# Kernel tuning notes

Hardware: AMD Instinct MI355X
Metric: run time of the kernel (lower is better)

Reference implementation:

```python
import jax, jax.numpy as jnp
import numpy as np

B, T, C = 2, 2048, 1024
LAT = 256
N_HEAD = 16
HEAD_DIM = C // N_HEAD
SCALE = 1.0 / np.sqrt(HEAD_DIM).astype(np.float32)


def setup_inputs() -> dict:
    key = jax.random.key(0)
    ks = jax.random.split(key, 9)
    s_in = 0.02  # small init so softmax is well-conditioned
    return {
        "x": jax.random.normal(ks[0], (B, T, C), dtype=jnp.float32),
        "wq_lat": jax.random.normal(ks[1], (C, LAT), dtype=jnp.float32) * s_in,
        "wk_lat": jax.random.normal(ks[2], (C, LAT), dtype=jnp.float32) * s_in,
        "wv_lat": jax.random.normal(ks[3], (C, LAT), dtype=jnp.float32) * s_in,
        "wq_heads": jax.random.normal(ks[4], (LAT, C), dtype=jnp.float32) * s_in,
        "wk_heads": jax.random.normal(ks[5], (LAT, C), dtype=jnp.float32) * s_in,
        "wv_heads": jax.random.normal(ks[6], (LAT, C), dtype=jnp.float32) * s_in,
        "w_proj": jax.random.normal(ks[7], (C, C), dtype=jnp.float32) * s_in,
        "b_proj": jnp.zeros((C,), dtype=jnp.float32),
    }


def reference(x, wq_lat, wk_lat, wv_lat, wq_heads, wk_heads, wv_heads, w_proj, b_proj):
    Bx, Tx, Cx = x.shape
    # low-rank latent projections then up-projection to per-head q/k/v
    q = (x @ wq_lat) @ wq_heads  # [B,T,C]
    k = (x @ wk_lat) @ wk_heads
    v = (x @ wv_lat) @ wv_heads
    q = q.reshape(Bx, Tx, N_HEAD, HEAD_DIM).transpose(0, 2, 1, 3)  # [B,H,T,D]
    k = k.reshape(Bx, Tx, N_HEAD, HEAD_DIM).transpose(0, 2, 1, 3)
    v = v.reshape(Bx, Tx, N_HEAD, HEAD_DIM).transpose(0, 2, 1, 3)
    att = jnp.einsum("bhqd,bhkd->bhqk", q, k) * SCALE  # [B,H,T,T]
    causal = jnp.tril(jnp.ones((Tx, Tx), dtype=bool))
    att = jnp.where(causal[None, None], att, -jnp.inf)
    att = jax.nn.softmax(att, axis=-1)
    y = jnp.einsum("bhqk,bhkd->bhqd", att, v)  # [B,H,T,D]
    y = y.transpose(0, 2, 1, 3).reshape(Bx, Tx, Cx)
    return y @ w_proj + b_proj
```

## Files before the change

### kernel.cpp

```cpp
#include <hip/hip_runtime.h>

#define SCALE 0.125f
#define SL 0.18033688011112042f

typedef __bf16 bf16x8 __attribute__((ext_vector_type(8)));
typedef short short4v __attribute__((ext_vector_type(4)));
typedef unsigned short u16x4 __attribute__((ext_vector_type(4)));
typedef float f32x4 __attribute__((ext_vector_type(4)));
typedef unsigned int uint2v __attribute__((ext_vector_type(2)));

__device__ __forceinline__ unsigned short f2b(float f) {
  unsigned u = __float_as_uint(f);
  u += 0x7fffu + ((u >> 16) & 1u);
  return (unsigned short)(u >> 16);
}
__device__ __forceinline__ float ex2(float x) {
  float r;
  asm("v_exp_f32 %0, %1" : "=v"(r) : "v"(x));
  return r;
}

#define GLB(p) ((__attribute__((address_space(1))) void*)(void*)(p))
#define LDSP(p) ((__attribute__((address_space(3))) void*)(p))

__global__ __launch_bounds__(256) void prep(
    const float* __restrict__ x, const float* __restrict__ wq_lat,
    const float* __restrict__ wk_lat, const float* __restrict__ wv_lat,
    const float* __restrict__ wq_h, const float* __restrict__ wk_h,
    const float* __restrict__ wv_h, const float* __restrict__ w_proj,
    unsigned short* __restrict__ x_bf, unsigned short* __restrict__ wlatT,
    unsigned short* __restrict__ whT, unsigned short* __restrict__ wpT) {
  __shared__ float tile[32][33];
  const int blk = blockIdx.x, tid = threadIdx.x;
  if (blk < 1024) {
    int i = blk * 256 + tid;
#pragma unroll
    for (int j = 0; j < 4; j++) {
      float4 v = ((const float4*)x)[i + j * 262144];
      u16x4 p;
      p.x = f2b(v.x); p.y = f2b(v.y); p.z = f2b(v.z); p.w = f2b(v.w);
      ((u16x4*)x_bf)[i + j * 262144] = p;
    }
  } else if (blk < 1792) {
    int idx = blk - 1024;
    int z = idx >> 8, rem = idx & 255;
    const float* wsrc = z == 0 ? wq_lat : (z == 1 ? wk_lat : wv_lat);
    unsigned short* o = wlatT + z * 262144;
    int c0 = (rem & 7) * 32, r0 = (rem >> 3) * 32;
    int tx = tid & 31, ty = tid >> 5;
#pragma unroll
    for (int i = 0; i < 32; i += 8) tile[ty + i][tx] = wsrc[(r0 + ty + i) * 256 + c0 + tx];
    __syncthreads();
#pragma unroll
    for (int i = 0; i < 32; i += 8) o[(c0 + ty + i) * 1024 + r0 + tx] = f2b(tile[tx][ty + i]);
  } else if (blk < 2560) {
    int idx = blk - 1792;
    int z = idx >> 8, rem = idx & 255;
    const float* wsrc = z == 0 ? wq_h : (z == 1 ? wk_h : wv_h);
    unsigned short* o = whT + z * 262144;
    int c0 = (rem & 31) * 32, r0 = (rem >> 5) * 32;
    int tx = tid & 31, ty = tid >> 5;
#pragma unroll
    for (int i = 0; i < 32; i += 8) tile[ty + i][tx] = wsrc[(r0 + ty + i) * 1024 + c0 + tx];
    __syncthreads();
#pragma unroll
    for (int i = 0; i < 32; i += 8) o[(c0 + ty + i) * 256 + r0 + tx] = f2b(tile[tx][ty + i]);
  } else {
    int idx = blk - 2560;
    int c0 = (idx & 31) * 32, r0 = (idx >> 5) * 32;
    int tx = tid & 31, ty = tid >> 5;
#pragma unroll
    for (int i = 0; i < 32; i += 8) tile[ty + i][tx] = w_proj[(r0 + ty + i) * 1024 + c0 + tx];
    __syncthreads();
#pragma unroll
    for (int i = 0; i < 32; i += 8) wpT[(c0 + ty + i) * 1024 + r0 + tx] = f2b(tile[tx][ty + i]);
  }
}

template <int MODE>
__global__ __launch_bounds__(256) void gemm_bt(
    const unsigned short* __restrict__ A0, const unsigned short* __restrict__ A1,
    const unsigned short* __restrict__ A2,
    const unsigned short* __restrict__ B0, const unsigned short* __restrict__ B1,
    const unsigned short* __restrict__ B2,
    void* __restrict__ C0, void* __restrict__ C1, void* __restrict__ C2,
    const float* __restrict__ bias, int M, int N, int K) {
  int bx, by, z;
  if (gridDim.y == 1) {
    const int lin = blockIdx.x;
    const int xcd = lin & 7, slot = lin >> 3;
    by = xcd * 4 + (slot & 3);
    bx = slot >> 2;
    z = 0;
  } else {
    bx = blockIdx.x; by = blockIdx.y; z = blockIdx.z;
  }
  const unsigned short* A = z == 0 ? A0 : (z == 1 ? A1 : A2);
  const unsigned short* BT = z == 0 ? B0 : (z == 1 ? B1 : B2);
  void* C = z == 0 ? C0 : (z == 1 ? C1 : C2);

  __shared__ char smem[32768];

  const int t = threadIdx.x;
  const int n0 = bx * 128;
  const int m0 = by * 128;
  const int lane = t & 63;
  const int wid = t >> 6;
  const int wr = wid >> 1, wc = wid & 1;
  const int lo = lane & 15, g = lane >> 4;

  f32x4 acc[4][4];
#pragma unroll
  for (int i = 0; i < 4; i++)
#pragma unroll
    for (int j = 0; j < 4; j++) acc[i][j] = (f32x4){0.f, 0.f, 0.f, 0.f};

  const unsigned short* ga = A + (size_t)(m0 + (t >> 2)) * K + (t & 3) * 8;
  const unsigned short* gb = BT + (size_t)(n0 + (t >> 2)) * K + (t & 3) * 8;
  const size_t rowK64 = (size_t)64 * K;
  char* dA = smem + t * 16;
  char* dB = smem + 16384 + t * 16;
  const char* rA = smem + (wr * 64 + lo) * 64 + g * 16;
  const char* rB = smem + 16384 + (wc * 64 + lo) * 64 + g * 16;

#define STGB(D, kof)                                                                     \
  __builtin_amdgcn_global_load_lds(GLB(ga + (kof)), LDSP(dA + (D)*8192), 16, 0, 0);      \
  __builtin_amdgcn_global_load_lds(GLB(ga + rowK64 + (kof)), LDSP(dA + (D)*8192 + 4096), 16, 0, 0); \
  __builtin_amdgcn_global_load_lds(GLB(gb + (kof)), LDSP(dB + (D)*8192), 16, 0, 0);      \
  __builtin_amdgcn_global_load_lds(GLB(gb + rowK64 + (kof)), LDSP(dB + (D)*8192 + 4096), 16, 0, 0);

#define COMPB(D)                                                                         \
  {                                                                                      \
    bf16x8 af[4], bfr[4];                                                                \
    _Pragma("unroll") for (int i = 0; i < 4; i++) {                                      \
      af[i] = *(const bf16x8*)(rA + (D)*8192 + i * 1024);                                \
      bfr[i] = *(const bf16x8*)(rB + (D)*8192 + i * 1024);                               \
    }                                                                                    \
    __builtin_amdgcn_s_setprio(1);                                                       \
    _Pragma("unroll") for (int i = 0; i < 4; i++)                                        \
    _Pragma("unroll") for (int j = 0; j < 4; j++)                                        \
        acc[i][j] = __builtin_amdgcn_mfma_f32_16x16x32_bf16(af[i], bfr[j], acc[i][j], 0, 0, 0); \
    __builtin_amdgcn_s_setprio(0);                                                       \
  }

  STGB(0, 0);
  asm volatile("s_waitcnt vmcnt(0)" ::: "memory");
  __builtin_amdgcn_s_barrier();
  for (int k0 = 0; k0 < K; k0 += 64) {
    if (k0 + 32 < K) { STGB(1, k0 + 32); }
    COMPB(0);
    asm volatile("s_waitcnt vmcnt(0)" ::: "memory");
    __builtin_amdgcn_s_barrier();
    if (k0 + 64 < K) { STGB(0, k0 + 64); }
    COMPB(1);
    asm volatile("s_waitcnt vmcnt(0)" ::: "memory");
    __builtin_amdgcn_s_barrier();
  }
#undef STGB
#undef COMPB

  if constexpr (MODE == 2) {
    float* Cf = (float*)C;
#pragma unroll
    for (int i = 0; i < 4; i++) {
      int row0 = m0 + wr * 64 + i * 16 + g * 4;
#pragma unroll
      for (int j = 0; j < 4; j++) {
        int col = n0 + wc * 64 + j * 16 + lo;
        float bv = bias[col];
#pragma unroll
        for (int r = 0; r < 4; r++) Cf[(size_t)(row0 + r) * N + col] = acc[i][j][r] + bv;
      }
    }
  } else {
    unsigned short* Cb = (unsigned short*)C;
#pragma unroll
    for (int i = 0; i < 4; i++) {
      int row0 = m0 + wr * 64 + i * 16 + g * 4;
#pragma unroll
      for (int j = 0; j < 4; j++) {
        int col = n0 + wc * 64 + j * 16 + lo;
#pragma unroll
        for (int r = 0; r < 4; r++) Cb[(size_t)(row0 + r) * N + col] = f2b(acc[i][j][r]);
      }
    }
  }
}

__global__ __launch_bounds__(512) void gemm_up8(const unsigned short* __restrict__ A,
                                                const unsigned short* __restrict__ BT,
                                                unsigned short* __restrict__ Qo,
                                                unsigned short* __restrict__ Ko,
                                                unsigned short* __restrict__ Vo) {
  __shared__ char smem[131072];

  const int t = threadIdx.x;
  const int lane = t & 63;
  const int wid = t >> 6;
  const int wr = wid >> 2, wc = wid & 3;
  const int lo = lane & 15, g = lane >> 4;
  const int lin = blockIdx.x;
  const int xcd = lin & 7;
  const int slot = lin >> 3;
  const int by = (xcd << 1) | (slot >= 12 ? 1 : 0);
  const int bx = slot >= 12 ? slot - 12 : slot;
  const int m0 = by * 256;
  const int z = bx >> 2;
  const int ncb = (bx & 3) * 256;
  const unsigned short* Az = A + (size_t)z * 1048576;
  const unsigned short* Bz = BT + (size_t)z * 262144;

  const int slog8 = (((t & 3) ^ ((t >> 2) & 3) ^ (((t >> 4) & 1) << 1)) << 3);
  const unsigned short *aS00, *aS01, *aS10, *aS11, *bS00, *bS01, *bS10, *bS11;
  {
    const int r = t >> 2;
    aS00 = Az + (size_t)(m0 + r) * 256 + slog8;
    aS01 = Az + (size_t)(m0 + r + 128) * 256 + slog8;
    aS10 = aS00 + 32;
    aS11 = aS01 + 32;
    bS00 = Bz + (size_t)(ncb + r) * 256 + slog8;
    bS01 = Bz + (size_t)(ncb + r + 128) * 256 + slog8;
    bS10 = bS00 + 32;
    bS11 = bS01 + 32;
  }
  char* dA0 = smem + t * 16;
  char* dA1 = smem + 16384 + t * 16;
  char* dB0 = smem + 32768 + t * 16;
  char* dB1 = smem + 49152 + t * 16;

  const int slotA = ((g ^ (lo & 3) ^ (((lo >> 2) & 1) << 1)) << 4);
  const char* aR = smem + (wr * 128 + lo) * 64 + slotA;
  const char* bR = smem + 32768 + (wc * 64 + lo) * 64 + slotA;

  f32x4 acc[8][4];
#pragma unroll
  for (int i = 0; i < 8; i++)
#pragma unroll
    for (int j = 0; j < 4; j++) acc[i][j] = (f32x4){0.f, 0.f, 0.f, 0.f};

#define STG(p0, p1, dst, D)                                                              \
  __builtin_amdgcn_global_load_lds(GLB(p0), LDSP(dst + (D)*65536), 16, 0, 0);            \
  __builtin_amdgcn_global_load_lds(GLB(p1), LDSP(dst + (D)*65536 + 8192), 16, 0, 0);     \
  p0 += 64; p1 += 64;

#define MF16(FRB, af, bf)                                                                \
  __builtin_amdgcn_s_setprio(1);                                                         \
  _Pragma("unroll") for (int i = 0; i < 4; i++)                                          \
  _Pragma("unroll") for (int j = 0; j < 4; j++)                                          \
      acc[(FRB) + i][j] = __builtin_amdgcn_mfma_f32_16x16x32_bf16(af[i], bf[j],          \
                                                                  acc[(FRB) + i][j], 0, 0, 0); \
  __builtin_amdgcn_s_setprio(0);

#define TILE(D, S)                                                                       \
  {                                                                                      \
    bf16x8 af[4], bf[4];                                                                 \
    _Pragma("unroll") for (int j = 0; j < 4; j++)                                        \
        bf[j] = *(const bf16x8*)(bR + (D)*65536 + j * 1024);                             \
    _Pragma("unroll") for (int i = 0; i < 4; i++)                                        \
        af[i] = *(const bf16x8*)(aR + (D)*65536 + i * 1024);                             \
    if (S) { STG(aS00, aS01, dA0, (D) ^ 1); }                                            \
    __builtin_amdgcn_s_barrier();                                                        \
    MF16(0, af, bf);                                                                     \
    __builtin_amdgcn_s_barrier();                                                        \
    _Pragma("unroll") for (int i = 0; i < 4; i++)                                        \
        af[i] = *(const bf16x8*)(aR + (D)*65536 + (4 + i) * 1024);                       \
    if (S) { STG(bS00, bS01, dB0, (D) ^ 1); }                                            \
    __builtin_amdgcn_s_barrier();                                                        \
    MF16(4, af, bf);                                                                     \
    if (S) { asm volatile("s_waitcnt vmcnt(4)" ::: "memory"); }                          \
    else   { asm volatile("s_waitcnt vmcnt(0)" ::: "memory"); }                          \
    __builtin_amdgcn_s_barrier();                                                        \
    _Pragma("unroll") for (int j = 0; j < 4; j++)                                        \
        bf[j] = *(const bf16x8*)(bR + (D)*65536 + 16384 + j * 1024);                     \
    _Pragma("unroll") for (int i = 0; i < 4; i++)                                        \
        af[i] = *(const bf16x8*)(aR + (D)*65536 + 16384 + i * 1024);                     \
    if (S) { STG(aS10, aS11, dA1, (D) ^ 1); }                                            \
    __builtin_amdgcn_s_barrier();                                                        \
    MF16(0, af, bf);                                                                     \
    __builtin_amdgcn_s_barrier();                                                        \
    _Pragma("unroll") for (int i = 0; i < 4; i++)                                        \
        af[i] = *(const bf16x8*)(aR + (D)*65536 + 16384 + (4 + i) * 1024);               \
    if (S) { STG(bS10, bS11, dB1, (D) ^ 1); }                                            \
    __builtin_amdgcn_s_barrier();                                                        \
    MF16(4, af, bf);                                                                     \
    if (S) { asm volatile("s_waitcnt vmcnt(4)" ::: "memory"); }                          \
    __builtin_amdgcn_s_barrier();                                                        \
  }

  { STG(aS00, aS01, dA0, 0); }
  { STG(bS00, bS01, dB0, 0); }
  { STG(aS10, aS11, dA1, 0); }
  { STG(bS10, bS11, dB1, 0); }
  asm volatile("s_waitcnt vmcnt(0)" ::: "memory");
  __builtin_amdgcn_s_barrier();

  TILE(0, 1);
  TILE(1, 1);
  TILE(0, 1);
  TILE(1, 0);

#undef TILE
#undef MF16
#undef STG

  if (z < 2) {
    unsigned short* Cb = z == 0 ? Qo : Ko;
    const float scl = z == 0 ? SL : 1.0f;
#pragma unroll
    for (int fr = 0; fr < 8; fr++) {
      int row0 = m0 + wr * 128 + fr * 16 + g * 4;
#pragma unroll
      for (int fc = 0; fc < 4; fc++) {
        int col = ncb + wc * 64 + fc * 16 + lo;
#pragma unroll
        for (int r = 0; r < 4; r++) Cb[(size_t)(row0 + r) * 1024 + col] = f2b(acc[fr][fc][r] * scl);
      }
    }
  } else {
#pragma unroll
    for (int fr = 0; fr < 8; fr++) {
      int row0 = m0 + wr * 128 + fr * 16 + g * 4;
      int bb = row0 >> 11, tloc = row0 & 2047;
#pragma unroll
      for (int fc = 0; fc < 4; fc++) {
        int col = ncb + wc * 64 + fc * 16 + lo;
        u16x4 pk;
#pragma unroll
        for (int r = 0; r < 4; r++) pk[r] = f2b(acc[fr][fc][r]);
        *(u16x4*)&Vo[((size_t)(bb * 1024) + col) * 2048 + tloc] = pk;
      }
    }
  }
}

__global__ __launch_bounds__(256) void attn_fwd(const unsigned short* __restrict__ Q,
                                                const unsigned short* __restrict__ K,
                                                const unsigned short* __restrict__ VT,
                                                unsigned short* __restrict__ Y) {
  __shared__ char smem[32768];

  const int tid = threadIdx.x;
  const int w = tid >> 6;
  const int lane = tid & 63;
  const int lo = lane & 15, g = lane >> 4;
  const int lo7 = lo & 7;
  const int bid = blockIdx.x;
  const int bh = bid & 31;
  const int code = bid >> 5;
  const int qq = code >> 3, kk = code & 7;
  const int chunk = qq == 0 ? 31 - kk : (qq == 1 ? 16 + kk : (qq == 2 ? 15 - kk : kk));
  const int b = bh >> 4, h = bh & 15;
  const int q0 = chunk * 64 + w * 16;

  const unsigned short* Qb = Q + (size_t)(b * 2048) * 1024 + h * 64;
  const unsigned short* Kb = K + (size_t)(b * 2048) * 1024 + h * 64;
  const unsigned short* Vb = VT + (size_t)((b * 16 + h) * 64) * 2048;

  bf16x8 qf0 = *(const bf16x8*)(Qb + (size_t)(q0 + lo) * 1024 + g * 8);
  bf16x8 qf1 = *(const bf16x8*)(Qb + (size_t)(q0 + lo) * 1024 + 32 + g * 8);

  const f32x4 z4 = (f32x4){0.f, 0.f, 0.f, 0.f};
  f32x4 acc[4];
#pragma unroll
  for (int dt = 0; dt < 4; dt++) acc[dt] = z4;
  float lrun = 0.f;
  const int nt = chunk + 1;

  const int koff = lo * 128 + ((g ^ lo7) << 4);
  char* kb0 = smem + koff;
  char* kb1 = smem + (koff ^ 64);
  const int voff = lo * 128 + ((g ^ ((lo7 & 1) << 1)) << 3) + ((lo7 >> 1) << 5);
  char* vq0 = smem + 16384 + voff;
  char* vq1 = smem + 16384 + (voff ^ 32);
  char* vq2 = smem + 16384 + (voff ^ 64);
  char* vq3 = smem + 16384 + (voff ^ 96);

  const int r0s = tid >> 3, c0s = (tid & 7) ^ (r0s & 7);
  const unsigned short* sk0 = Kb + (size_t)r0s * 1024 + c0s * 8;
  const unsigned short* sk1 = sk0 + (size_t)32 * 1024;
  const unsigned short* sv0 = Vb + (size_t)r0s * 2048 + c0s * 8;
  const unsigned short* sv1 = sv0 + (size_t)32 * 2048;
  char* dk0 = smem + tid * 16;
  char* dk1 = smem + 4096 + tid * 16;
  char* dv0 = smem + 16384 + tid * 16;
  char* dv1 = smem + 20480 + tid * 16;

#define STAGE(BUF)                                                                        \
  __builtin_amdgcn_global_load_lds(GLB(sk0), LDSP(dk0 + (BUF)*8192), 16, 0, 0);           \
  __builtin_amdgcn_global_load_lds(GLB(sk1), LDSP(dk1 + (BUF)*8192), 16, 0, 0);           \
  __builtin_amdgcn_global_load_lds(GLB(sv0), LDSP(dv0 + (BUF)*8192), 16, 0, 0);           \
  __builtin_amdgcn_global_load_lds(GLB(sv1), LDSP(dv1 + (BUF)*8192), 16, 0, 0);           \
  sk0 += 65536; sk1 += 65536; sv0 += 64; sv1 += 64;

#define COMPUTE(k0v, BUF, MASKED)                                                         \
  {                                                                                       \
    bf16x8 kfA[4], kfB[4];                                                                \
    _Pragma("unroll") for (int kvf = 0; kvf < 4; kvf++) {                                 \
      kfA[kvf] = *(const bf16x8*)(kb0 + (BUF)*8192 + kvf * 2048);                         \
      kfB[kvf] = *(const bf16x8*)(kb1 + (BUF)*8192 + kvf * 2048);                         \
    }                                                                                     \
    short4v vf[4][4];                                                                     \
    _Pragma("unroll") for (int kvf = 0; kvf < 4; kvf++) {                                 \
      const char* vp = kvf == 0 ? vq0 : (kvf == 1 ? vq1 : (kvf == 2 ? vq2 : vq3));        \
      _Pragma("unroll") for (int dt = 0; dt < 4; dt++)                                    \
          vf[dt][kvf] = *(const short4v*)(vp + (BUF)*8192 + dt * 2048);                   \
    }                                                                                     \
    f32x4 st[4];                                                                          \
    __builtin_amdgcn_s_setprio(1);                                                        \
    _Pragma("unroll") for (int kvf = 0; kvf < 4; kvf++) {                                 \
      st[kvf] = __builtin_amdgcn_mfma_f32_16x16x32_bf16(kfA[kvf], qf0, z4, 0, 0, 0);      \
      st[kvf] = __builtin_amdgcn_mfma_f32_16x16x32_bf16(kfB[kvf], qf1, st[kvf], 0, 0, 0); \
    }                                                                                     \
    __builtin_amdgcn_s_setprio(0);                                                        \
    if (MASKED) {                                                                         \
      const int qg = q0 + lo;                                                             \
      _Pragma("unroll") for (int kvf = 0; kvf < 4; kvf++)                                 \
      _Pragma("unroll") for (int r = 0; r < 4; r++) {                                     \
        int tk = (k0v) + kvf * 16 + g * 4 + r;                                            \
        if (tk > qg) st[kvf][r] = -3.0e38f;                                               \
      }                                                                                   \
    }                                                                                     \
    __builtin_amdgcn_s_setprio(1);                                                        \
    _Pragma("unroll") for (int kvf = 0; kvf < 4; kvf++) {                                 \
      float p0 = ex2(st[kvf][0]);                                                         \
      float p1 = ex2(st[kvf][1]);                                                         \
      float p2 = ex2(st[kvf][2]);                                                         \
      float p3 = ex2(st[kvf][3]);                                                         \
      lrun += (p0 + p1) + (p2 + p3);                                                      \
      uint2v pw;                                                                          \
      pw.x = __builtin_amdgcn_perm(__float_as_uint(p1), __float_as_uint(p0), 0x07060302u); \
      pw.y = __builtin_amdgcn_perm(__float_as_uint(p3), __float_as_uint(p2), 0x07060302u); \
      short4v pb = __builtin_bit_cast(short4v, pw);                                       \
      _Pragma("unroll") for (int dt = 0; dt < 4; dt++)                                    \
          acc[dt] = __builtin_amdgcn_mfma_f32_16x16x16bf16_1k(vf[dt][kvf], pb,            \
                                                              acc[dt], 0, 0, 0);          \
    }                                                                                     \
    __builtin_amdgcn_s_setprio(0);                                                        \
  }

  STAGE(0);
  __syncthreads();
  int t = 0;
  for (; t + 2 <= nt - 1; t += 2) {
    STAGE(1);
    COMPUTE(t * 64, 0, false);
    __syncthreads();
    STAGE(0);
    COMPUTE(t * 64 + 64, 1, false);
    __syncthreads();
  }
  if (t < nt - 1) {
    STAGE(1);
    COMPUTE(t * 64, 0, false);
    __syncthreads();
    COMPUTE(t * 64 + 64, 1, true);
  } else {
    COMPUTE(t * 64, 0, true);
  }

  {
    float l = lrun;
    l += __shfl_xor(l, 16);
    l += __shfl_xor(l, 32);
    float inv = 1.0f / l;
    unsigned short* yp = Y + (size_t)(b * 2048 + q0 + lo) * 1024 + h * 64;
#pragma unroll
    for (int dt = 0; dt < 4; dt++) {
      float y0 = acc[dt][0] * inv, y1 = acc[dt][1] * inv;
      float y2 = acc[dt][2] * inv, y3 = acc[dt][3] * inv;
      uint2v pw;
      pw.x = __builtin_amdgcn_perm(__float_as_uint(y1), __float_as_uint(y0), 0x07060302u);
      pw.y = __builtin_amdgcn_perm(__float_as_uint(y3), __float_as_uint(y2), 0x07060302u);
      *(uint2v*)&yp[dt * 16 + g * 4] = pw;
    }
  }
#undef STAGE
#undef COMPUTE
}

extern "C" void kernel_launch(void* const* d_in, const int* in_sizes, int n_in,
                              void* d_out, int out_size, void* d_ws, size_t ws_size,
                              hipStream_t stream) {
  const float* x = (const float*)d_in[0];
  const float* wq_lat = (const float*)d_in[1];
  const float* wk_lat = (const float*)d_in[2];
  const float* wv_lat = (const float*)d_in[3];
  const float* wq_h = (const float*)d_in[4];
  const float* wk_h = (const float*)d_in[5];
  const float* wv_h = (const float*)d_in[6];
  const float* w_proj = (const float*)d_in[7];
  const float* b_proj = (const float*)d_in[8];
  float* out = (float*)d_out;

  char* ws = (char*)d_ws;
  unsigned short* x_bf = (unsigned short*)(ws + 0);
  unsigned short* wlatT = (unsigned short*)(ws + 8388608);
  unsigned short* whT = (unsigned short*)(ws + 9961472);
  unsigned short* wpT = (unsigned short*)(ws + 11534336);
  unsigned short* lat = (unsigned short*)(ws + 13631488);
  unsigned short* q_bf = (unsigned short*)(ws + 19922944);
  unsigned short* k_bf = (unsigned short*)(ws + 28311552);
  unsigned short* vT = (unsigned short*)(ws + 36700160);
  unsigned short* y_bf = (unsigned short*)(ws + 45088768);

  prep<<<3584, 256, 0, stream>>>(x, wq_lat, wk_lat, wv_lat, wq_h, wk_h, wv_h, w_proj,
                                 x_bf, wlatT, whT, wpT);

  gemm_bt<0><<<dim3(2, 32, 3), 256, 0, stream>>>(
      x_bf, x_bf, x_bf, wlatT, wlatT + 262144, wlatT + 524288,
      lat, lat + 1048576, lat + 2097152, nullptr, 4096, 256, 1024);

  gemm_up8<<<192, 512, 0, stream>>>(lat, whT, q_bf, k_bf, vT);

  attn_fwd<<<1024, 256, 0, stream>>>(q_bf, k_bf, vT, y_bf);

  gemm_bt<2><<<256, 256, 0, stream>>>(
      y_bf, y_bf, y_bf, wpT, wpT, wpT, out, out, out, b_proj, 4096, 1024, 1024);
}
```

Baseline: 98.80 us.

## Triple-buffer K/V tiles in attention with explicit vmcnt waits and simpler block order

Changes the attention kernel from double to triple buffering of K/V tiles in LDS (48KB), keeping two tiles in flight ahead of compute. Explicit s_waitcnt vmcnt counts plus raw s_barrier replace the full __syncthreads after each stage, so loads can overlap more deeply with MFMA work. The block-to-chunk mapping becomes a plain descending order (largest causal chunk first) instead of the interleaved pattern. More LDS per block may lower occupancy, and the rotating buffer pointers add some scalar overhead.

Result: no change. 98.88 us (+0.1%).

```diff
diff --git a/kernel.cpp b/kernel.cpp
--- a/kernel.cpp
+++ b/kernel.cpp
@@ -337,7 +337,7 @@
                                                 const unsigned short* __restrict__ K,
                                                 const unsigned short* __restrict__ VT,
                                                 unsigned short* __restrict__ Y) {
-  __shared__ char smem[32768];
+  __shared__ char smem[49152];
 
   const int tid = threadIdx.x;
   const int w = tid >> 6;
@@ -346,9 +346,7 @@
   const int lo7 = lo & 7;
   const int bid = blockIdx.x;
   const int bh = bid & 31;
-  const int code = bid >> 5;
-  const int qq = code >> 3, kk = code & 7;
-  const int chunk = qq == 0 ? 31 - kk : (qq == 1 ? 16 + kk : (qq == 2 ? 15 - kk : kk));
+  const int chunk = 31 - (bid >> 5);
   const int b = bh >> 4, h = bh & 15;
   const int q0 = chunk * 64 + w * 16;
 
@@ -366,44 +364,43 @@
   float lrun = 0.f;
   const int nt = chunk + 1;
 
-  const int koff = lo * 128 + ((g ^ lo7) << 4);
-  char* kb0 = smem + koff;
-  char* kb1 = smem + (koff ^ 64);
+  const int kA = lo * 128 + ((g ^ lo7) << 4);
+  const int kB = kA ^ 64;
   const int voff = lo * 128 + ((g ^ ((lo7 & 1) << 1)) << 3) + ((lo7 >> 1) << 5);
-  char* vq0 = smem + 16384 + voff;
-  char* vq1 = smem + 16384 + (voff ^ 32);
-  char* vq2 = smem + 16384 + (voff ^ 64);
-  char* vq3 = smem + 16384 + (voff ^ 96);
+  const int v0o = 8192 + voff;
+  const int v1o = 8192 + (voff ^ 32);
+  const int v2o = 8192 + (voff ^ 64);
+  const int v3o = 8192 + (voff ^ 96);
 
   const int r0s = tid >> 3, c0s = (tid & 7) ^ (r0s & 7);
   const unsigned short* sk0 = Kb + (size_t)r0s * 1024 + c0s * 8;
   const unsigned short* sk1 = sk0 + (size_t)32 * 1024;
   const unsigned short* sv0 = Vb + (size_t)r0s * 2048 + c0s * 8;
   const unsigned short* sv1 = sv0 + (size_t)32 * 2048;
-  char* dk0 = smem + tid * 16;
-  char* dk1 = smem + 4096 + tid * 16;
-  char* dv0 = smem + 16384 + tid * 16;
-  char* dv1 = smem + 20480 + tid * 16;
-
-#define STAGE(BUF)                                                                        \
-  __builtin_amdgcn_global_load_lds(GLB(sk0), LDSP(dk0 + (BUF)*8192), 16, 0, 0);           \
-  __builtin_amdgcn_global_load_lds(GLB(sk1), LDSP(dk1 + (BUF)*8192), 16, 0, 0);           \
-  __builtin_amdgcn_global_load_lds(GLB(sv0), LDSP(dv0 + (BUF)*8192), 16, 0, 0);           \
-  __builtin_amdgcn_global_load_lds(GLB(sv1), LDSP(dv1 + (BUF)*8192), 16, 0, 0);           \
+  const int dst = tid * 16;
+
+  char* cbuf = smem;
+  char* sbuf = smem + 32768;
+
+#define STAGE(SB)                                                                         \
+  __builtin_amdgcn_global_load_lds(GLB(sk0), LDSP(SB + dst), 16, 0, 0);                   \
+  __builtin_amdgcn_global_load_lds(GLB(sk1), LDSP(SB + dst + 4096), 16, 0, 0);            \
+  __builtin_amdgcn_global_load_lds(GLB(sv0), LDSP(SB + dst + 8192), 16, 0, 0);            \
+  __builtin_amdgcn_global_load_lds(GLB(sv1), LDSP(SB + dst + 12288), 16, 0, 0);           \
   sk0 += 65536; sk1 += 65536; sv0 += 64; sv1 += 64;
 
-#define COMPUTE(k0v, BUF, MASKED)                                                         \
+#define COMPUTE(CB, k0v, MASKED)                                                          \
   {                                                                                       \
     bf16x8 kfA[4], kfB[4];                                                                \
     _Pragma("unroll") for (int kvf = 0; kvf < 4; kvf++) {                                 \
-      kfA[kvf] = *(const bf16x8*)(kb0 + (BUF)*8192 + kvf * 2048);                         \
-      kfB[kvf] = *(const bf16x8*)(kb1 + (BUF)*8192 + kvf * 2048);                         \
+      kfA[kvf] = *(const bf16x8*)(CB + kA + kvf * 2048);                                  \
+      kfB[kvf] = *(const bf16x8*)(CB + kB + kvf * 2048);                                  \
     }                                                                                     \
     short4v vf[4][4];                                                                     \
     _Pragma("unroll") for (int kvf = 0; kvf < 4; kvf++) {                                 \
-      const char* vp = kvf == 0 ? vq0 : (kvf == 1 ? vq1 : (kvf == 2 ? vq2 : vq3));        \
+      const int vo = kvf == 0 ? v0o : (kvf == 1 ? v1o : (kvf == 2 ? v2o : v3o));          \
       _Pragma("unroll") for (int dt = 0; dt < 4; dt++)                                    \
-          vf[dt][kvf] = *(const short4v*)(vp + (BUF)*8192 + dt * 2048);                   \
+          vf[dt][kvf] = *(const short4v*)(CB + vo + dt * 2048);                           \
     }                                                                                     \
     f32x4 st[4];                                                                          \
     __builtin_amdgcn_s_setprio(1);                                                        \
@@ -438,24 +435,27 @@
     __builtin_amdgcn_s_setprio(0);                                                        \
   }
 
-  STAGE(0);
-  __syncthreads();
-  int t = 0;
-  for (; t + 2 <= nt - 1; t += 2) {
-    STAGE(1);
-    COMPUTE(t * 64, 0, false);
-    __syncthreads();
-    STAGE(0);
-    COMPUTE(t * 64 + 64, 1, false);
-    __syncthreads();
-  }
-  if (t < nt - 1) {
-    STAGE(1);
-    COMPUTE(t * 64, 0, false);
-    __syncthreads();
-    COMPUTE(t * 64 + 64, 1, true);
-  } else {
-    COMPUTE(t * 64, 0, true);
+  STAGE(smem);
+  if (nt > 1) { STAGE((smem + 16384)); }
+
+  for (int t = 0; t < nt; ++t) {
+    if (t + 2 < nt) {
+      STAGE(sbuf);
+      sbuf += 16384;
+      if (sbuf == smem + 49152) sbuf = smem;
+    }
+    if (t + 2 < nt) {
+      asm volatile("s_waitcnt vmcnt(8)" ::: "memory");
+    } else if (t + 1 < nt) {
+      asm volatile("s_waitcnt vmcnt(4)" ::: "memory");
+    } else {
+      asm volatile("s_waitcnt vmcnt(0)" ::: "memory");
+    }
+    __builtin_amdgcn_s_barrier();
+    COMPUTE(cbuf, t * 64, (t == nt - 1));
+    cbuf += 16384;
+    if (cbuf == smem + 49152) cbuf = smem;
+    __builtin_amdgcn_s_barrier();
   }
 
   {
```
